# Optimization experiments

Measured on AMD Instinct MI355X. Metric: run time of the kernel, lower is better.

Reference implementation:

```python
import jax, jax.numpy as jnp
import numpy as np

N_NODES = 100000
NEG_SLOPE = 0.2


def gat_layer(x, src, dst, W, al, ar, b):
    # x: [N, F_in]; src/dst: [E]; W: [F_in, F_out]; al/ar/b: [F_out]
    h = x @ W                                  # [N, F_out]
    el = h @ al                                # [N] per-src attention term
    er = h @ ar                                # [N] per-dst attention term
    e = jax.nn.leaky_relu(el[src] + er[dst], NEG_SLOPE)   # [E]
    # edge softmax over incoming edges of each dst node (numerically stable)
    mx = jax.ops.segment_max(e, dst, num_segments=N_NODES)
    mx = jnp.where(jnp.isfinite(mx), mx, 0.0)  # zero-in-degree guard
    ex = jnp.exp(e - mx[dst])
    denom = jax.ops.segment_sum(ex, dst, num_segments=N_NODES)
    alpha = ex / jnp.maximum(denom[dst], 1e-9)             # [E]
    out = jax.ops.segment_sum(alpha[:, None] * h[src], dst, num_segments=N_NODES)
    return out + b


def setup_inputs() -> dict:
    key = jax.random.key(0)
    ks = jax.random.split(key, 11)
    N, E, F_in, F_h = N_NODES, 1600000, 128, 64
    x = jax.random.normal(ks[0], (N, F_in), dtype=jnp.float32)
    src = jax.random.randint(ks[1], (E,), 0, N, dtype=jnp.int32)
    dst = jax.random.randint(ks[2], (E,), 0, N, dtype=jnp.int32)
    s1 = 1.0 / np.sqrt(F_in)
    s2 = 1.0 / np.sqrt(F_h)
    W1 = jax.random.normal(ks[3], (F_in, F_h), dtype=jnp.float32) * s1
    al1 = jax.random.normal(ks[4], (F_h,), dtype=jnp.float32) * s2
    ar1 = jax.random.normal(ks[5], (F_h,), dtype=jnp.float32) * s2
    b1 = jnp.zeros((F_h,), dtype=jnp.float32)
    W2 = jax.random.normal(ks[6], (F_h, F_h), dtype=jnp.float32) * s2
    al2 = jax.random.normal(ks[7], (F_h,), dtype=jnp.float32) * s2
    ar2 = jax.random.normal(ks[8], (F_h,), dtype=jnp.float32) * s2
    b2 = jnp.zeros((F_h,), dtype=jnp.float32)
    return {"x": x, "src": src, "dst": dst, "W1": W1, "al1": al1, "ar1": ar1,
            "b1": b1, "W2": W2, "al2": al2, "ar2": ar2, "b2": b2}


def reference(x, src, dst, W1, al1, ar1, b1, W2, al2, ar2, b2):
    h = gat_layer(x, src, dst, W1, al1, ar1, b1)   # conv1, head squeezed
    h = jax.nn.relu(h)                              # dropout = identity (eval)
    h = gat_layer(h, src, dst, W2, al2, ar2, b2)   # conv2
    return h
```

## Files before the change

### kernel.cpp

```cpp
#include <hip/hip_runtime.h>
#include <hip/hip_fp16.h>

#define NNODES 100000
#define NEG_SLOPE 0.2f
#define NBK 49
#define BKSHIFT 11
#define BKMASK 2047
#define BCAP 35328
#define B1 4096

typedef _Float16 f16x8 __attribute__((ext_vector_type(8)));
typedef float f32x4 __attribute__((ext_vector_type(4)));


__global__ void k_init(int* __restrict__ gcur, int* __restrict__ offs, int N, int E) {
    int t = threadIdx.x;
    if (t < NBK) gcur[t] = t * BCAP;
    if (t == NBK) offs[N] = E;
}


__global__ __launch_bounds__(256) void k_bin(const int* __restrict__ src,
                                             const int* __restrict__ dst,
                                             int* __restrict__ gcur,
                                             int* __restrict__ be, int E) {
    __shared__ int lcnt[NBK], lbase[NBK], lcur[NBK];
    int t = threadIdx.x;
    int base = blockIdx.x * B1;
    if (t < NBK) lcnt[t] = 0;
    __syncthreads();
#pragma unroll
    for (int j = 0; j < B1 / 256; ++j) {
        int e = base + j * 256 + t;
        if (e < E) atomicAdd(&lcnt[dst[e] >> BKSHIFT], 1);
    }
    __syncthreads();
    if (t < NBK) { lbase[t] = atomicAdd(&gcur[t], lcnt[t]); lcur[t] = 0; }
    __syncthreads();
#pragma unroll
    for (int j = 0; j < B1 / 256; ++j) {
        int e = base + j * 256 + t;
        if (e < E) {
            int d = dst[e];
            int bk = d >> BKSHIFT;
            int p = lbase[bk] + atomicAdd(&lcur[bk], 1);
            be[p] = (src[e] << BKSHIFT) | (d & BKMASK);
        }
    }
}


__global__ __launch_bounds__(256, 4) void k_gemm1sc(
    const float* __restrict__ x, const float* __restrict__ W,
    const float* __restrict__ al, const float* __restrict__ ar,
    __half* __restrict__ h, float* __restrict__ el, float* __restrict__ er,
    int N, const int* __restrict__ gcur, const int* __restrict__ be,
    int* __restrict__ offs, int* __restrict__ csr, int E) {

    __shared__ float4 SMEM[2048];
    int t = threadIdx.x;

    if ((int)blockIdx.x < NBK) {
        int* I = (int*)SMEM;
        int* cnt = I;
        int* sb  = I + 2048;
        int b = blockIdx.x;
        int mycnt = gcur[b] - b * BCAP;
        int ebase = b * BCAP;

        for (int i = t; i < 2048; i += 256) cnt[i] = 0;
        if (t == 0) I[2560] = 0;
        __syncthreads();
        for (int i = t; i < mycnt; i += 256) atomicAdd(&cnt[be[ebase + i] & BKMASK], 1);
        if (t < 64) {
            int v = (t < b) ? gcur[t] - t * BCAP : 0;
#pragma unroll
            for (int o = 32; o; o >>= 1) v += __shfl_xor(v, o);
            if (t == 0) I[2560] = v;
        }
        __syncthreads();

        int loc[8]; int s = 0;
#pragma unroll
        for (int i = 0; i < 8; ++i) { loc[i] = s; s += cnt[8 * t + i]; }
        sb[t] = s;
        __syncthreads();
        int pi = 0;
        for (int d = 1; d < 256; d <<= 1) {
            int po = pi ^ 1;
            sb[po * 256 + t] = sb[pi * 256 + t] + (t >= d ? sb[pi * 256 + t - d] : 0);
            pi = po;
            __syncthreads();
        }
        int bas = I[2560] + sb[pi * 256 + t] - s;

        int node0 = (b << BKSHIFT) + 8 * t;
#pragma unroll
        for (int i = 0; i < 8; ++i) {
            int node = node0 + i;
            if (node < N) offs[node] = bas + loc[i];
        }
        __syncthreads();
#pragma unroll
        for (int i = 0; i < 8; ++i) cnt[8 * t + i] = bas + loc[i];
        __syncthreads();
        for (int i = t; i < mycnt; i += 256) {
            int v = be[ebase + i];
            int p = atomicAdd(&cnt[v & BKMASK], 1);
            csr[p] = v >> BKSHIFT;
        }
        return;
    }

    char* A  = (char*)SMEM;
    char* Bw = (char*)SMEM + 16384;
    int row0 = ((int)blockIdx.x - NBK) * 64;

    for (int i = t; i < 2048; i += 256) {
        int r = i >> 5, c4 = i & 31;
        int rr = row0 + r; if (rr > N - 1) rr = N - 1;
        float4 v = *(const float4*)(x + (size_t)rr * 128 + c4 * 4);
        int byte = r * 256 + ((c4 * 8) ^ ((r & 7) << 4));
        *(__half2*)(A + byte)     = __floats2half2_rn(v.x, v.y);
        *(__half2*)(A + byte + 4) = __floats2half2_rn(v.z, v.w);
    }
    for (int i = t; i < 2048; i += 256) {
        int k = i >> 4, c4 = (i & 15) * 4;
        float4 v = *(const float4*)(W + k * 64 + c4);
        int kb = k * 2;
        *(__half*)(Bw + (c4 + 0) * 256 + (kb ^ (((c4 + 0) & 7) << 4))) = __float2half(v.x);
        *(__half*)(Bw + (c4 + 1) * 256 + (kb ^ (((c4 + 1) & 7) << 4))) = __float2half(v.y);
        *(__half*)(Bw + (c4 + 2) * 256 + (kb ^ (((c4 + 2) & 7) << 4))) = __float2half(v.z);
        *(__half*)(Bw + (c4 + 3) * 256 + (kb ^ (((c4 + 3) & 7) << 4))) = __float2half(v.w);
    }
    __syncthreads();

    int w = t >> 6, l = t & 63, g = l >> 4, c = l & 15;
    int swz = (c & 7) << 4;
    const char* Ar = A + (w * 16 + c) * 256;

    f32x4 acc[4];
#pragma unroll
    for (int t2 = 0; t2 < 4; ++t2) acc[t2] = (f32x4){0.f, 0.f, 0.f, 0.f};
#pragma unroll
    for (int kk = 0; kk < 4; ++kk) {
        int kb = kk * 64 + g * 16;
        f16x8 av = *(const f16x8*)(Ar + (kb ^ swz));
#pragma unroll
        for (int t2 = 0; t2 < 4; ++t2) {
            f16x8 bv = *(const f16x8*)(Bw + (t2 * 16 + c) * 256 + (kb ^ swz));
            acc[t2] = __builtin_amdgcn_mfma_f32_16x16x32_f16(av, bv, acc[t2], 0, 0, 0);
        }
    }

    float alv[4], arv[4];
#pragma unroll
    for (int t2 = 0; t2 < 4; ++t2) { alv[t2] = al[t2 * 16 + c]; arv[t2] = ar[t2 * 16 + c]; }
#pragma unroll
    for (int r = 0; r < 4; ++r) {
        float e1 = 0.f, e2 = 0.f;
#pragma unroll
        for (int t2 = 0; t2 < 4; ++t2) {
            e1 = fmaf(acc[t2][r], alv[t2], e1);
            e2 = fmaf(acc[t2][r], arv[t2], e2);
        }
#pragma unroll
        for (int o = 1; o < 16; o <<= 1) { e1 += __shfl_xor(e1, o); e2 += __shfl_xor(e2, o); }
        int row = row0 + w * 16 + 4 * g + r;
        if (row < N) {
            if (c == 0) { el[row] = e1; er[row] = e2; }
#pragma unroll
            for (int t2 = 0; t2 < 4; ++t2)
                h[(size_t)row * 64 + t2 * 16 + c] = __float2half(acc[t2][r]);
        }
    }
}


__global__ __launch_bounds__(256, 4) void k_gemm2(
    const __half* __restrict__ xin, const float* __restrict__ W,
    const float* __restrict__ al, const float* __restrict__ ar,
    __half* __restrict__ h, float* __restrict__ el, float* __restrict__ er, int N) {

    __shared__ float4 AlR[512];
    __shared__ float4 WtR[512];
    char* A = (char*)AlR;
    char* Bw = (char*)WtR;
    int tid = threadIdx.x;
    int row0 = blockIdx.x * 64;

    for (int i = tid; i < 512; i += 256) {
        int r = i >> 3, o = i & 7;
        int rr = row0 + r; if (rr > N - 1) rr = N - 1;
        float4 v = *(const float4*)(xin + (size_t)rr * 64 + o * 8);
        *(float4*)(A + r * 128 + ((o * 16) ^ ((r & 7) << 4))) = v;
    }
    for (int i = tid; i < 1024; i += 256) {
        int k = i >> 4, c4 = (i & 15) * 4;
        float4 v = *(const float4*)(W + k * 64 + c4);
        int kb = k * 2;
        *(__half*)(Bw + (c4 + 0) * 128 + (kb ^ (((c4 + 0) & 7) << 4))) = __float2half(v.x);
        *(__half*)(Bw + (c4 + 1) * 128 + (kb ^ (((c4 + 1) & 7) << 4))) = __float2half(v.y);
        *(__half*)(Bw + (c4 + 2) * 128 + (kb ^ (((c4 + 2) & 7) << 4))) = __float2half(v.z);
        *(__half*)(Bw + (c4 + 3) * 128 + (kb ^ (((c4 + 3) & 7) << 4))) = __float2half(v.w);
    }
    __syncthreads();

    int w = tid >> 6, l = tid & 63, g = l >> 4, c = l & 15;
    int swz = (c & 7) << 4;
    const char* Ar = A + (w * 16 + c) * 128;

    f32x4 acc[4];
#pragma unroll
    for (int t2 = 0; t2 < 4; ++t2) acc[t2] = (f32x4){0.f, 0.f, 0.f, 0.f};
#pragma unroll
    for (int kk = 0; kk < 2; ++kk) {
        int kb = kk * 64 + g * 16;
        f16x8 av = *(const f16x8*)(Ar + (kb ^ swz));
#pragma unroll
        for (int t2 = 0; t2 < 4; ++t2) {
            f16x8 bv = *(const f16x8*)(Bw + (t2 * 16 + c) * 128 + (kb ^ swz));
            acc[t2] = __builtin_amdgcn_mfma_f32_16x16x32_f16(av, bv, acc[t2], 0, 0, 0);
        }
    }

    float alv[4], arv[4];
#pragma unroll
    for (int t2 = 0; t2 < 4; ++t2) { alv[t2] = al[t2 * 16 + c]; arv[t2] = ar[t2 * 16 + c]; }
#pragma unroll
    for (int r = 0; r < 4; ++r) {
        float e1 = 0.f, e2 = 0.f;
#pragma unroll
        for (int t2 = 0; t2 < 4; ++t2) {
            e1 = fmaf(acc[t2][r], alv[t2], e1);
            e2 = fmaf(acc[t2][r], arv[t2], e2);
        }
#pragma unroll
        for (int o = 1; o < 16; o <<= 1) { e1 += __shfl_xor(e1, o); e2 += __shfl_xor(e2, o); }
        int row = row0 + w * 16 + 4 * g + r;
        if (row < N) {
            if (c == 0) { el[row] = e1; er[row] = e2; }
#pragma unroll
            for (int t2 = 0; t2 < 4; ++t2)
                h[(size_t)row * 64 + t2 * 16 + c] = __float2half(acc[t2][r]);
        }
    }
}


__device__ inline float2 h2_to_f2(float bits) {
    return __half22float2(__builtin_bit_cast(__half2, bits));
}

template <bool OUT_HALF>
__global__ __launch_bounds__(256) void k_agg(const __half* __restrict__ h,
                                             const float* __restrict__ el,
                                             const float* __restrict__ er,
                                             const float* __restrict__ b,
                                             const int* __restrict__ offs,
                                             const int* __restrict__ csr_src,
                                             void* __restrict__ outp, int N, int relu) {
    int wave = threadIdx.x >> 6, lane = threadIdx.x & 63;
    int n = blockIdx.x * 4 + wave;
    if (n >= N) return;

    int beg = offs[n], end = offs[n + 1];
    int deg = end - beg;
    float ern = er[n];

    int g = lane >> 4;
    int fl = lane & 15;
    float4 accv = make_float4(0.f, 0.f, 0.f, 0.f);
    const size_t foff = 4 * (size_t)fl;

    if (deg <= 64) {
        int sidx = 0;
        float e = -1e30f;
        if (lane < deg) {
            sidx = csr_src[beg + lane];
            e = el[sidx] + ern;
            e = e > 0.f ? e : NEG_SLOPE * e;
        }
        float m = e;
#pragma unroll
        for (int o = 32; o; o >>= 1) m = fmaxf(m, __shfl_xor(m, o));
        float p = (lane < deg) ? __expf(e - m) : 0.f;
        float s = p;
#pragma unroll
        for (int o = 32; o; o >>= 1) s += __shfl_xor(s, o);
        float a = p * (1.f / fmaxf(s, 1e-9f));

        int iters = (deg + 3) >> 2;
        int pair = iters >> 1;
        int i = g;
        for (int t2 = 0; t2 < pair; ++t2, i += 8) {
            int s0 = __shfl(sidx, i), s1 = __shfl(sidx, i + 4);
            float w0 = __shfl(a, i), w1 = __shfl(a, i + 4);
            float2 r0 = *(const float2*)(h + (size_t)s0 * 64 + foff);
            float2 r1 = *(const float2*)(h + (size_t)s1 * 64 + foff);
            float2 f00 = h2_to_f2(r0.x), f01 = h2_to_f2(r0.y);
            float2 f10 = h2_to_f2(r1.x), f11 = h2_to_f2(r1.y);
            accv.x = fmaf(w0, f00.x, accv.x); accv.y = fmaf(w0, f00.y, accv.y);
            accv.z = fmaf(w0, f01.x, accv.z); accv.w = fmaf(w0, f01.y, accv.w);
            accv.x = fmaf(w1, f10.x, accv.x); accv.y = fmaf(w1, f10.y, accv.y);
            accv.z = fmaf(w1, f11.x, accv.z); accv.w = fmaf(w1, f11.y, accv.w);
        }
        if (iters & 1) {
            int s0 = __shfl(sidx, i);
            float w0 = __shfl(a, i);
            float2 r0 = *(const float2*)(h + (size_t)s0 * 64 + foff);
            float2 f00 = h2_to_f2(r0.x), f01 = h2_to_f2(r0.y);
            accv.x = fmaf(w0, f00.x, accv.x); accv.y = fmaf(w0, f00.y, accv.y);
            accv.z = fmaf(w0, f01.x, accv.z); accv.w = fmaf(w0, f01.y, accv.w);
        }
    } else {
        float m = -1e30f;
        for (int i = beg + lane; i < end; i += 64) {
            float e = el[csr_src[i]] + ern;
            e = e > 0.f ? e : NEG_SLOPE * e;
            m = fmaxf(m, e);
        }
#pragma unroll
        for (int o = 32; o; o >>= 1) m = fmaxf(m, __shfl_xor(m, o));
        float s = 0.f;
        for (int i = beg + lane; i < end; i += 64) {
            float e = el[csr_src[i]] + ern;
            e = e > 0.f ? e : NEG_SLOPE * e;
            s += __expf(e - m);
        }
#pragma unroll
        for (int o = 32; o; o >>= 1) s += __shfl_xor(s, o);
        float inv = 1.f / fmaxf(s, 1e-9f);

        for (int i = g; i < deg; i += 4) {
            int s0 = csr_src[beg + i];
            float e = el[s0] + ern;
            e = e > 0.f ? e : NEG_SLOPE * e;
            float w0 = __expf(e - m) * inv;
            float2 r0 = *(const float2*)(h + (size_t)s0 * 64 + foff);
            float2 f00 = h2_to_f2(r0.x), f01 = h2_to_f2(r0.y);
            accv.x = fmaf(w0, f00.x, accv.x); accv.y = fmaf(w0, f00.y, accv.y);
            accv.z = fmaf(w0, f01.x, accv.z); accv.w = fmaf(w0, f01.y, accv.w);
        }
    }

#pragma unroll
    for (int o = 16; o <= 32; o <<= 1) {
        accv.x += __shfl_xor(accv.x, o);
        accv.y += __shfl_xor(accv.y, o);
        accv.z += __shfl_xor(accv.z, o);
        accv.w += __shfl_xor(accv.w, o);
    }

    if (lane < 16) {
        float4 bv = *(const float4*)(b + foff);
        float ox = accv.x + bv.x, oy = accv.y + bv.y;
        float oz = accv.z + bv.z, ow = accv.w + bv.w;
        if (relu) {
            ox = fmaxf(ox, 0.f); oy = fmaxf(oy, 0.f);
            oz = fmaxf(oz, 0.f); ow = fmaxf(ow, 0.f);
        }
        if (OUT_HALF) {
            __half* oh = (__half*)outp + (size_t)n * 64 + foff;
            *(__half2*)(oh)     = __floats2half2_rn(ox, oy);
            *(__half2*)(oh + 2) = __floats2half2_rn(oz, ow);
        } else {
            *(float4*)((float*)outp + (size_t)n * 64 + foff) = make_float4(ox, oy, oz, ow);
        }
    }
}


extern "C" void kernel_launch(void* const* d_in, const int* in_sizes, int n_in,
                              void* d_out, int out_size, void* d_ws, size_t ws_size,
                              hipStream_t stream) {
    const float* x   = (const float*)d_in[0];
    const int*   src = (const int*)d_in[1];
    const int*   dst = (const int*)d_in[2];
    const float* W1  = (const float*)d_in[3];
    const float* al1 = (const float*)d_in[4];
    const float* ar1 = (const float*)d_in[5];
    const float* b1  = (const float*)d_in[6];
    const float* W2  = (const float*)d_in[7];
    const float* al2 = (const float*)d_in[8];
    const float* ar2 = (const float*)d_in[9];
    const float* b2  = (const float*)d_in[10];
    float* out = (float*)d_out;

    const int N = NNODES;
    const int E = in_sizes[1];

    __half* h    = (__half*)d_ws;
    __half* hmid = h + (size_t)N * 64;
    int*    be   = (int*)(hmid + (size_t)N * 64);
    int*    csr  = be + (size_t)NBK * BCAP;
    float*  el   = (float*)(csr + E);
    float*  er   = el + N;
    int*    offs = (int*)(er + N);
    int*    gcur = offs + N + 1;

    int nbBin = (E + B1 - 1) / B1;
    int nbG   = (N + 63) / 64;
    int nbR   = (N + 3) / 4;

    k_init<<<1, 64, 0, stream>>>(gcur, offs, N, E);
    k_bin<<<nbBin, 256, 0, stream>>>(src, dst, gcur, be, E);
    k_gemm1sc<<<NBK + nbG, 256, 0, stream>>>(x, W1, al1, ar1, h, el, er, N,
                                             gcur, be, offs, csr, E);
    k_agg<true><<<nbR, 256, 0, stream>>>(h, el, er, b1, offs, csr, hmid, N, 1);
    k_gemm2<<<nbG, 256, 0, stream>>>(hmid, W2, al2, ar2, h, el, er, N);
    k_agg<false><<<nbR, 256, 0, stream>>>(h, el, er, b2, offs, csr, out, N, 0);
}
```

Measured before the change: 221.0 us.

## Split CSR scatter into separate offset kernel and 8-way sliced scatter blocks

Moves the per-bucket count and prefix-scan that computes node offsets into a new k_offs kernel. The scatter part of k_gemm1sc is then split into 8 slices per bucket (392 blocks instead of 49), each re-reading the whole bucket but only placing edges whose local destination falls in its 256-node slice. This is meant to fix the load imbalance where 49 long-running scatter blocks dominated the fused GEMM launch. The cost is one extra kernel launch and 8x redundant reads of the binned edge array. k_bin also keeps dst values in registers so the second pass does not reload them.

```diff
diff --git a/kernel.cpp b/kernel.cpp
--- a/kernel.cpp
+++ b/kernel.cpp
@@ -8,6 +8,7 @@
 #define BKMASK 2047
 #define BCAP 35328
 #define B1 4096
+#define NSL (NBK * 8)
 
 typedef _Float16 f16x8 __attribute__((ext_vector_type(8)));
 typedef float f32x4 __attribute__((ext_vector_type(4)));
@@ -29,23 +30,70 @@
     int base = blockIdx.x * B1;
     if (t < NBK) lcnt[t] = 0;
     __syncthreads();
-#pragma unroll
-    for (int j = 0; j < B1 / 256; ++j) {
+    int dreg[16];
+#pragma unroll
+    for (int j = 0; j < 16; ++j) {
         int e = base + j * 256 + t;
-        if (e < E) atomicAdd(&lcnt[dst[e] >> BKSHIFT], 1);
+        dreg[j] = (e < E) ? dst[e] : -1;
+        if (e < E) atomicAdd(&lcnt[dreg[j] >> BKSHIFT], 1);
     }
     __syncthreads();
     if (t < NBK) { lbase[t] = atomicAdd(&gcur[t], lcnt[t]); lcur[t] = 0; }
     __syncthreads();
 #pragma unroll
-    for (int j = 0; j < B1 / 256; ++j) {
+    for (int j = 0; j < 16; ++j) {
         int e = base + j * 256 + t;
         if (e < E) {
-            int d = dst[e];
+            int d = dreg[j];
             int bk = d >> BKSHIFT;
             int p = lbase[bk] + atomicAdd(&lcur[bk], 1);
             be[p] = (src[e] << BKSHIFT) | (d & BKMASK);
         }
+    }
+}
+
+
+__global__ __launch_bounds__(256) void k_offs(const int* __restrict__ be,
+                                              const int* __restrict__ gcur,
+                                              int* __restrict__ offs, int N) {
+    __shared__ int cnt[2048];
+    __shared__ int sb[2][256];
+    __shared__ int rbeg;
+    int B = blockIdx.x, t = threadIdx.x;
+    int mycnt = gcur[B] - B * BCAP;
+    int ebase = B * BCAP;
+
+    for (int i = t; i < 2048; i += 256) cnt[i] = 0;
+    if (t == 0) rbeg = 0;
+    __syncthreads();
+    for (int i = t; i < mycnt; i += 256) atomicAdd(&cnt[be[ebase + i] & BKMASK], 1);
+    if (t < 64) {
+        int v = (t < B) ? gcur[t] - t * BCAP : 0;
+#pragma unroll
+        for (int o = 32; o; o >>= 1) v += __shfl_xor(v, o);
+        if (t == 0) rbeg = v;
+    }
+    __syncthreads();
+
+    int loc[8], s = 0;
+#pragma unroll
+    for (int i = 0; i < 8; ++i) { loc[i] = s; s += cnt[8 * t + i]; }
+    sb[0][t] = s;
+    __syncthreads();
+    int pi = 0;
+    for (int d = 1; d < 256; d <<= 1) {
+        int po = pi ^ 1;
+        sb[po][t] = sb[pi][t] + (t >= d ? sb[pi][t - d] : 0);
+        pi = po;
+        __syncthreads();
+    }
+    int bas = rbeg + sb[pi][t] - s;
+
+    int node0 = (B << BKSHIFT) + 8 * t;
+#pragma unroll
+    for (int i = 0; i < 8; ++i) {
+        int node = node0 + i;
+        if (node < N) offs[node] = bas + loc[i];
     }
 }
 
@@ -55,66 +103,34 @@
     const float* __restrict__ al, const float* __restrict__ ar,
     __half* __restrict__ h, float* __restrict__ el, float* __restrict__ er,
     int N, const int* __restrict__ gcur, const int* __restrict__ be,
-    int* __restrict__ offs, int* __restrict__ csr, int E) {
+    const int* __restrict__ offs, int* __restrict__ csr, int E) {
 
     __shared__ float4 SMEM[2048];
     int t = threadIdx.x;
 
-    if ((int)blockIdx.x < NBK) {
-        int* I = (int*)SMEM;
-        int* cnt = I;
-        int* sb  = I + 2048;
+    if ((int)blockIdx.x < NSL) {
+        int* cur = (int*)SMEM;
         int b = blockIdx.x;
-        int mycnt = gcur[b] - b * BCAP;
-        int ebase = b * BCAP;
-
-        for (int i = t; i < 2048; i += 256) cnt[i] = 0;
-        if (t == 0) I[2560] = 0;
-        __syncthreads();
-        for (int i = t; i < mycnt; i += 256) atomicAdd(&cnt[be[ebase + i] & BKMASK], 1);
-        if (t < 64) {
-            int v = (t < b) ? gcur[t] - t * BCAP : 0;
-#pragma unroll
-            for (int o = 32; o; o >>= 1) v += __shfl_xor(v, o);
-            if (t == 0) I[2560] = v;
-        }
-        __syncthreads();
-
-        int loc[8]; int s = 0;
-#pragma unroll
-        for (int i = 0; i < 8; ++i) { loc[i] = s; s += cnt[8 * t + i]; }
-        sb[t] = s;
-        __syncthreads();
-        int pi = 0;
-        for (int d = 1; d < 256; d <<= 1) {
-            int po = pi ^ 1;
-            sb[po * 256 + t] = sb[pi * 256 + t] + (t >= d ? sb[pi * 256 + t - d] : 0);
-            pi = po;
-            __syncthreads();
-        }
-        int bas = I[2560] + sb[pi * 256 + t] - s;
-
-        int node0 = (b << BKSHIFT) + 8 * t;
-#pragma unroll
-        for (int i = 0; i < 8; ++i) {
-            int node = node0 + i;
-            if (node < N) offs[node] = bas + loc[i];
-        }
-        __syncthreads();
-#pragma unroll
-        for (int i = 0; i < 8; ++i) cnt[8 * t + i] = bas + loc[i];
+        int B = b >> 3, sl = b & 7;
+        int mycnt = gcur[B] - B * BCAP;
+        int ebase = B * BCAP;
+        int node = (B << BKSHIFT) + sl * 256 + t;
+        cur[t] = (node < N) ? offs[node] : 0;
         __syncthreads();
         for (int i = t; i < mycnt; i += 256) {
             int v = be[ebase + i];
-            int p = atomicAdd(&cnt[v & BKMASK], 1);
-            csr[p] = v >> BKSHIFT;
+            int loc = v & BKMASK;
+            if ((loc >> 8) == sl) {
+                int p = atomicAdd(&cur[loc & 255], 1);
+                csr[p] = v >> BKSHIFT;
+            }
         }
         return;
     }
 
     char* A  = (char*)SMEM;
     char* Bw = (char*)SMEM + 16384;
-    int row0 = ((int)blockIdx.x - NBK) * 64;
+    int row0 = ((int)blockIdx.x - NSL) * 64;
 
     for (int i = t; i < 2048; i += 256) {
         int r = i >> 5, c4 = i & 31;
@@ -405,7 +421,8 @@
 
     k_init<<<1, 64, 0, stream>>>(gcur, offs, N, E);
     k_bin<<<nbBin, 256, 0, stream>>>(src, dst, gcur, be, E);
-    k_gemm1sc<<<NBK + nbG, 256, 0, stream>>>(x, W1, al1, ar1, h, el, er, N,
+    k_offs<<<NBK, 256, 0, stream>>>(be, gcur, offs, N);
+    k_gemm1sc<<<NSL + nbG, 256, 0, stream>>>(x, W1, al1, ar1, h, el, er, N,
                                              gcur, be, offs, csr, E);
     k_agg<true><<<nbR, 256, 0, stream>>>(h, el, er, b1, offs, csr, hmid, N, 1);
     k_gemm2<<<nbG, 256, 0, stream>>>(hmid, W2, al2, ar2, h, el, er, N);
```

Result: slower. 225.8 us (+2.2%).
